# Performance work log

Measured on AMD Instinct MI355X. Metric: run time of the kernel, lower is better.

Reference implementation:

```python
import jax, jax.numpy as jnp
import numpy as np

C2D, C3D = 256, 128
IA, IB = C2D // 2, C3D // 2  # inter channels: 128, 64
B, H, W = 4, 64, 64


def _conv1x1(x, w, b):
    # x: [B,Cin,H,W], w: [Cout,Cin], b: [Cout]
    return jnp.einsum('oc,bchw->bohw', w, x) + b[None, :, None, None]


def _cross_attn(Q, K, V):
    # Q,K,V: [B,C,H,W] (same C); full HWxHW attention as in the torch code
    Bs, C, h, w = Q.shape
    q = Q.reshape(Bs, C, h * w)
    k = K.reshape(Bs, C, K.shape[2] * K.shape[3])
    v = V.reshape(Bs, C, V.shape[2] * V.shape[3])
    attn = jnp.einsum('bcn,bcm->bnm', q, k) * (C ** -0.5)  # [B,N,M]
    attn = jax.nn.softmax(attn, axis=-1)
    out = jnp.einsum('bnm,bcm->bcn', attn, v)
    return out.reshape(Bs, C, h, w)


def setup_inputs() -> dict:
    key = jax.random.key(0)
    ks = jax.random.split(key, 20)
    def n(k, shape, scale=0.02):
        return jax.random.normal(k, shape, dtype=jnp.float32) * scale
    inp = {
        'features_2d': jax.random.normal(ks[0], (B, C2D, H, W), dtype=jnp.float32),
        'features_3d': jax.random.normal(ks[1], (B, C3D, H, W), dtype=jnp.float32),
        # stream A: Q from 2d, K/V from 3d, all mapped to IA channels
        'wqA': n(ks[2], (IA, C2D)), 'bqA': jnp.zeros((IA,), jnp.float32),
        'wkA': n(ks[3], (IA, C3D)), 'bkA': jnp.zeros((IA,), jnp.float32),
        'wvA': n(ks[4], (IA, C3D)), 'bvA': jnp.zeros((IA,), jnp.float32),
        'wpA': n(ks[5], (C2D, IA)), 'bpA': jnp.zeros((C2D,), jnp.float32),
        # stream B: Q from 3d, K/V from 2d, all mapped to IB channels
        'wqB': n(ks[6], (IB, C3D)), 'bqB': jnp.zeros((IB,), jnp.float32),
        'wkB': n(ks[7], (IB, C2D)), 'bkB': jnp.zeros((IB,), jnp.float32),
        'wvB': n(ks[8], (IB, C2D)), 'bvB': jnp.zeros((IB,), jnp.float32),
        'wpB': n(ks[9], (C3D, IB)), 'bpB': jnp.zeros((C3D,), jnp.float32),
    }
    return inp


def reference(features_2d, features_3d,
              wqA, bqA, wkA, bkA, wvA, bvA, wpA, bpA,
              wqB, bqB, wkB, bkB, wvB, bvB, wpB, bpB):
    Q_A = _conv1x1(features_2d, wqA, bqA)
    K_A = _conv1x1(features_3d, wkA, bkA)
    V_A = _conv1x1(features_3d, wvA, bvA)
    x_2D = features_2d + _conv1x1(_cross_attn(Q_A, K_A, V_A), wpA, bpA)

    Q_B = _conv1x1(features_3d, wqB, bqB)
    K_B = _conv1x1(features_2d, wkB, bkB)
    V_B = _conv1x1(features_2d, wvB, bvB)
    x_3D = features_3d + _conv1x1(_cross_attn(Q_B, K_B, V_B), wpB, bpB)
    return (x_2D, x_3D)
```

## Files before the change

### kernel.cpp

```cpp
#include <hip/hip_runtime.h>
#include <hip/hip_bf16.h>
#include <math.h>

typedef __bf16 bf16_t;
typedef __bf16 bf16x8 __attribute__((ext_vector_type(8)));
typedef float f32x4 __attribute__((ext_vector_type(4)));
typedef float f32x16 __attribute__((ext_vector_type(16)));
typedef unsigned u32x2 __attribute__((ext_vector_type(2)));

#define NPOS 4096
#define LOG2E 1.4426950408889634f

__device__ __forceinline__ f32x4 mfma16(bf16x8 a, bf16x8 b, f32x4 c) {
    return __builtin_amdgcn_mfma_f32_16x16x32_bf16(a, b, c, 0, 0, 0);
}
__device__ __forceinline__ f32x16 mfma32(bf16x8 a, bf16x8 b, f32x16 c) {
    return __builtin_amdgcn_mfma_f32_32x32x16_bf16(a, b, c, 0, 0, 0);
}

typedef __attribute__((address_space(1))) const unsigned gas_u32;
typedef __attribute__((address_space(3))) unsigned las_u32;
__device__ __forceinline__ void gl_lds16(const char* g, char* l) {
    __builtin_amdgcn_global_load_lds((gas_u32*)g, (las_u32*)l, 16, 0, 0);
}

__device__ __forceinline__ float fexp2(float x) {
    float r; asm("v_exp_f32 %0, %1" : "=v"(r) : "v"(x)); return r;
}

#define BARC(N) do {                                                          \
    asm volatile("s_waitcnt vmcnt(" #N ") lgkmcnt(0)" ::: "memory");          \
    __builtin_amdgcn_sched_barrier(0);                                        \
    __builtin_amdgcn_s_barrier();                                             \
    __builtin_amdgcn_sched_barrier(0);                                        \
} while (0)

template<int BYTES>
__device__ __forceinline__ void stG(char* lds, const char* g, int w, int lane) {
    constexpr int NC = BYTES / 4096;
#pragma unroll
    for (int c = 0; c < NC; ++c) {
        int j = (w * NC + c) * 1024 + lane * 16;
        gl_lds16(g + (j ^ (((j >> 8) & 15) << 4)), lds + j);
    }
}
template<int BYTES>
__device__ __forceinline__ void stV(char* lds, const char* g, int w, int lane) {
    constexpr int NC = BYTES / 4096;
#pragma unroll
    for (int c = 0; c < NC; ++c) {
        int j = (w * NC + c) * 1024 + lane * 16;
        int row = j >> 8;
        int col = (j & 255) ^ ((row & 15) << 4);
        int d = (row << 1) | (col >> 7);
        gl_lds16(g + (size_t)d * (NPOS * 2) + (col & 127), lds + j);
    }
}

template<int D>
__device__ __forceinline__ bf16x8 ldK(const char* lds, int key, int dbyte) {
    if constexpr (D == 128) {
        return *(const bf16x8*)(lds + key * 256 + (dbyte ^ ((key & 15) << 4)));
    } else {
        int row = key >> 1;
        int col = ((key & 1) << 7) | dbyte;
        return *(const bf16x8*)(lds + row * 256 + (col ^ ((row & 15) << 4)));
    }
}
__device__ __forceinline__ bf16x8 ldV(const char* lds, int d, int kbyte) {
    int row = d >> 1;
    int col = ((d & 1) << 7) | kbyte;
    return *(const bf16x8*)(lds + row * 256 + (col ^ ((row & 15) << 4)));
}

__device__ __forceinline__ unsigned pkbf(float a, float b) {
    union { bf16_t h[2]; unsigned u; } t;
    t.h[0] = (bf16_t)a; t.h[1] = (bf16_t)b;
    return t.u;
}
#define MKPA(sb, base) ({                                                   \
    unsigned a0_ = pkbf((sb)[(base)+0], (sb)[(base)+1]);                    \
    unsigned a1_ = pkbf((sb)[(base)+2], (sb)[(base)+3]);                    \
    unsigned a2_ = pkbf((sb)[(base)+4], (sb)[(base)+5]);                    \
    unsigned a3_ = pkbf((sb)[(base)+6], (sb)[(base)+7]);                    \
    u32x2 r0_ = __builtin_amdgcn_permlane32_swap(a2_, a0_, false, false);   \
    u32x2 r1_ = __builtin_amdgcn_permlane32_swap(a3_, a1_, false, false);   \
    union { unsigned u[4]; bf16x8 v; } pu_;                                 \
    pu_.u[0] = r0_.y; pu_.u[1] = r1_.y; pu_.u[2] = r0_.x; pu_.u[3] = r1_.x; \
    pu_.v; })

__global__ __launch_bounds__(256) void k_trw(const float* __restrict__ s2d,
                                             const float* __restrict__ s3d,
                                             bf16_t* __restrict__ d2d,
                                             bf16_t* __restrict__ d3d,
                                             const float* w0, const float* w1, const float* w2, const float* w3,
                                             const float* w4, const float* w5, const float* w6, const float* w7,
                                             bf16_t* wdst)
{
    __shared__ float tile[64][65];
    int bid = blockIdx.x, tid = threadIdx.x;
    if (bid >= 1536) {
        int i = (bid - 1536) * 256 + tid;
        if      (i <  32768) wdst[i] = (bf16_t)w0[i];
        else if (i <  49152) wdst[i] = (bf16_t)w1[i - 32768];
        else if (i <  65536) wdst[i] = (bf16_t)w2[i - 49152];
        else if (i <  98304) wdst[i] = (bf16_t)w3[i - 65536];
        else if (i < 106496) wdst[i] = (bf16_t)w4[i - 98304];
        else if (i < 122880) wdst[i] = (bf16_t)w5[i - 106496];
        else if (i < 139264) wdst[i] = (bf16_t)w6[i - 122880];
        else if (i < 147456) wdst[i] = (bf16_t)w7[i - 139264];
        return;
    }
    const float* src; bf16_t* dst; int C, b, c0, n0;
    if (bid < 1024) { src = s2d; dst = d2d; C = 256; b = bid >> 8; c0 = ((bid >> 6) & 3) << 6; n0 = (bid & 63) << 6; }
    else { int r = bid - 1024; src = s3d; dst = d3d; C = 128; b = r >> 7; c0 = ((r >> 6) & 1) << 6; n0 = (r & 63) << 6; }
    const float* sp = src + ((size_t)b * C + c0) * NPOS + n0;
#pragma unroll
    for (int i = 0; i < 16; i++) {
        int idx = tid + i * 256; int c = idx >> 6, n = idx & 63;
        tile[c][n] = sp[(size_t)c * NPOS + n];
    }
    __syncthreads();
    bf16_t* dp = dst + ((size_t)b * NPOS + n0) * C + c0;
#pragma unroll
    for (int i = 0; i < 16; i++) {
        int idx = tid + i * 256; int n = idx >> 6, c = idx & 63;
        dp[(size_t)n * C + c] = (bf16_t)tile[c][n];
    }
}

template<int K, int MQ, int MK, int MV>
__global__ __launch_bounds__(256, 2) void k_prod(const bf16_t* __restrict__ Xt,
                                                 const bf16_t* __restrict__ wq, const float* __restrict__ bq, float sq,
                                                 const bf16_t* __restrict__ wk, const float* __restrict__ bk,
                                                 const bf16_t* __restrict__ wv, const float* __restrict__ bv,
                                                 bf16_t* __restrict__ Qo, bf16_t* __restrict__ Ko, bf16_t* __restrict__ Vo)
{
    extern __shared__ char smem[];
    constexpr int RB = K * 2;
    int bid = blockIdx.x, tid = threadIdx.x;
    int b = bid >> 6, n0 = (bid & 63) << 6;
    int wave = tid >> 6, lane = tid & 63, g = lane >> 4, lr = lane & 15;

    const char* src = (const char*)(Xt + ((size_t)b * NPOS + n0) * K);
#pragma unroll
    for (int j0 = 0; j0 < 64 * RB; j0 += 4096) {
        int j = j0 + tid * 16;
        int row = j / RB;
        int col = j & (RB - 1);
        float4 v = *(const float4*)(src + (size_t)row * RB + col);
        *(float4*)(smem + row * RB + (col ^ ((row & 7) << 4))) = v;
    }
    __syncthreads();

    f32x4 aq[MQ / 16], ak[MK / 16], av[MV / 16];
#pragma unroll
    for (int ob = 0; ob < MQ / 16; ++ob) aq[ob] = f32x4{0.f,0.f,0.f,0.f};
#pragma unroll
    for (int ob = 0; ob < MK / 16; ++ob) ak[ob] = f32x4{0.f,0.f,0.f,0.f};
#pragma unroll
    for (int ob = 0; ob < MV / 16; ++ob) av[ob] = f32x4{0.f,0.f,0.f,0.f};
    int xrow = wave * 16 + lr;
#pragma unroll
    for (int ks = 0; ks < K / 32; ++ks) {
        bf16x8 xf = *(const bf16x8*)(smem + xrow * RB + ((((ks * 32 + g * 8) * 2)) ^ ((xrow & 7) << 4)));
#pragma unroll
        for (int ob = 0; ob < MQ / 16; ++ob) {
            bf16x8 wf = *(const bf16x8*)(wq + (size_t)(ob * 16 + lr) * K + ks * 32 + g * 8);
            aq[ob] = mfma16(xf, wf, aq[ob]);
        }
#pragma unroll
        for (int ob = 0; ob < MK / 16; ++ob) {
            bf16x8 wf = *(const bf16x8*)(wk + (size_t)(ob * 16 + lr) * K + ks * 32 + g * 8);
            ak[ob] = mfma16(xf, wf, ak[ob]);
        }
#pragma unroll
        for (int ob = 0; ob < MV / 16; ++ob) {
            bf16x8 wf = *(const bf16x8*)(wv + (size_t)(ob * 16 + lr) * K + ks * 32 + g * 8);
            av[ob] = mfma16(wf, xf, av[ob]);
        }
    }
#pragma unroll
    for (int ob = 0; ob < MQ / 16; ++ob) {
        int o = ob * 16 + lr;
        float bs = bq[o];
#pragma unroll
        for (int r = 0; r < 4; r++) {
            size_t n = (size_t)b * NPOS + n0 + wave * 16 + g * 4 + r;
            Qo[n * MQ + o] = (bf16_t)((aq[ob][r] + bs) * sq);
        }
    }
#pragma unroll
    for (int ob = 0; ob < MK / 16; ++ob) {
        int o = ob * 16 + lr;
        float bs = bk[o];
#pragma unroll
        for (int r = 0; r < 4; r++) {
            size_t n = (size_t)b * NPOS + n0 + wave * 16 + g * 4 + r;
            Ko[n * MK + o] = (bf16_t)(ak[ob][r] + bs);
        }
    }
#pragma unroll
    for (int ob = 0; ob < MV / 16; ++ob) {
#pragma unroll
        for (int r = 0; r < 4; r++) {
            int o = ob * 16 + g * 4 + r;
            size_t idx = ((size_t)b * MV + o) * NPOS + n0 + wave * 16 + lr;
            Vo[idx] = (bf16_t)(av[ob][r] + bv[o]);
        }
    }
}

template<int K, int M>
__global__ __launch_bounds__(256, 2) void k_out(const bf16_t* __restrict__ Xt,
                                                const bf16_t* __restrict__ W,
                                                const float* __restrict__ bias,
                                                const float* __restrict__ resid,
                                                float* __restrict__ outp,
                                                const float* __restrict__ lp)
{
    extern __shared__ char smem[];
    constexpr int RB = K * 2;
    int bid = blockIdx.x, tid = threadIdx.x;
    int b = bid >> 6, n0 = (bid & 63) << 6;
    int wave = tid >> 6, lane = tid & 63, g = lane >> 4, lr = lane & 15;

#pragma unroll
    for (int j0 = 0; j0 < 64 * RB; j0 += 4096) {
        int j = j0 + tid * 16;
        int row = j / RB;
        int colb = j & (RB - 1);
        size_t n = (size_t)b * NPOS + n0 + row;
        float l1 = lp[n], l2 = lp[16384 + n];
        float inv = 1.f / (l1 + l2);
        float w1 = l1 * inv, w2 = l2 * inv;
        bf16x8 o1 = *(const bf16x8*)(Xt + n * K + (colb >> 1));
        bf16x8 o2 = *(const bf16x8*)(Xt + (size_t)16384 * K + n * K + (colb >> 1));
        bf16x8 xv;
#pragma unroll
        for (int e = 0; e < 8; ++e) xv[e] = (bf16_t)(w1 * (float)o1[e] + w2 * (float)o2[e]);
        *(bf16x8*)(smem + row * RB + (colb ^ ((row & 7) << 4))) = xv;
    }
    __syncthreads();

    f32x4 acc[M / 16];
#pragma unroll
    for (int ob = 0; ob < M / 16; ++ob) acc[ob] = f32x4{0.f,0.f,0.f,0.f};
    int xrow = wave * 16 + lr;
#pragma unroll
    for (int ks = 0; ks < K / 32; ++ks) {
        bf16x8 xf = *(const bf16x8*)(smem + xrow * RB + ((((ks * 32 + g * 8) * 2)) ^ ((xrow & 7) << 4)));
#pragma unroll
        for (int ob = 0; ob < M / 16; ++ob) {
            bf16x8 wf = *(const bf16x8*)(W + (size_t)(ob * 16 + lr) * K + ks * 32 + g * 8);
            acc[ob] = mfma16(wf, xf, acc[ob]);
        }
    }
#pragma unroll
    for (int ob = 0; ob < M / 16; ++ob) {
#pragma unroll
        for (int r = 0; r < 4; r++) {
            int o = ob * 16 + g * 4 + r;
            size_t idx = ((size_t)b * M + o) * NPOS + n0 + wave * 16 + lr;
            outp[idx] = acc[ob][r] + bias[o] + resid[idx];
        }
    }
}

__device__ void attnA9(const bf16_t* __restrict__ Qt, const bf16_t* __restrict__ Kt,
                       const bf16_t* __restrict__ V, bf16_t* __restrict__ OtH,
                       float* __restrict__ lH, int b, int qblk, int half,
                       char* smem, int tid)
{
    char* Kb[3] = { smem, smem + 8192, smem + 16384 };
    char* Vb[2] = { smem + 24576, smem + 40960 };
    int w = tid >> 6, lane = tid & 63;
    int qcol = lane & 31, hi = lane >> 5;
    int q0 = qblk * 128 + w * 32;

    bf16x8 qf[8];
    const bf16_t* qp = Qt + ((size_t)b * NPOS + q0 + qcol) * 128 + hi * 8;
#pragma unroll
    for (int ks = 0; ks < 8; ++ks) qf[ks] = *(const bf16x8*)(qp + ks * 16);

    f32x16 acc[4];
#pragma unroll
    for (int cb = 0; cb < 4; ++cb)
#pragma unroll
        for (int i = 0; i < 16; ++i) acc[cb][i] = 0.f;
    float l_c = 0.f;

    const char* kg = (const char*)(Kt + (size_t)b * NPOS * 128) + (size_t)half * 64 * 8192;
    const char* vg = (const char*)(V + (size_t)b * 128 * NPOS) + (size_t)half * 32 * 128;

    stG<8192>(Kb[0], kg, w, lane);
    stV<16384>(Vb[0], vg, w, lane);
    stG<8192>(Kb[1], kg + 8192, w, lane);
    BARC(2);

    int rc = 0;
#pragma unroll 1
    for (int t2 = 0; t2 < 32; ++t2) {
        {
            int tK = 2 * t2 + 2; if (tK > 63) tK = 63;
            int st1 = t2 + 1;    if (st1 > 31) st1 = 31;
            int wn = rc ? rc - 1 : 2;
            stG<8192>(Kb[wn], kg + (size_t)tK * 8192, w, lane);
            stV<16384>(Vb[(t2 + 1) & 1], vg + (size_t)st1 * 128, w, lane);
            const char* Kc = Kb[rc];
            const char* Vc = Vb[t2 & 1];

            f32x16 s;
#pragma unroll
            for (int i = 0; i < 16; ++i) s[i] = 0.f;
            __builtin_amdgcn_s_setprio(1);
#pragma unroll
            for (int ks = 0; ks < 8; ++ks)
                s = mfma32(ldK<128>(Kc, qcol, ks * 32 + hi * 16), qf[ks], s);
            __builtin_amdgcn_s_setprio(0);
            float psum = 0.f;
#pragma unroll
            for (int i = 0; i < 16; ++i) { float e = fexp2(s[i]); s[i] = e; psum += e; }
            psum += __shfl_xor(psum, 32);
            l_c += psum;
            bf16x8 pa0 = MKPA(s, 0);
            bf16x8 pa1 = MKPA(s, 8);
            __builtin_amdgcn_s_setprio(1);
#pragma unroll
            for (int cb = 0; cb < 4; ++cb) {
                int d = cb * 32 + qcol;
                acc[cb] = mfma32(pa0, ldV(Vc, d, 0 + hi * 16), acc[cb]);
                acc[cb] = mfma32(pa1, ldV(Vc, d, 32 + hi * 16), acc[cb]);
            }
            __builtin_amdgcn_s_setprio(0);
            rc = (rc == 2) ? 0 : rc + 1;
            BARC(6);
        }
        {
            int tK = 2 * t2 + 3; if (tK > 63) tK = 63;
            int wn = rc ? rc - 1 : 2;
            stG<8192>(Kb[wn], kg + (size_t)tK * 8192, w, lane);
            const char* Kc = Kb[rc];
            const char* Vc = Vb[t2 & 1];

            f32x16 s;
#pragma unroll
            for (int i = 0; i < 16; ++i) s[i] = 0.f;
            __builtin_amdgcn_s_setprio(1);
#pragma unroll
            for (int ks = 0; ks < 8; ++ks)
                s = mfma32(ldK<128>(Kc, qcol, ks * 32 + hi * 16), qf[ks], s);
            __builtin_amdgcn_s_setprio(0);
            float psum = 0.f;
#pragma unroll
            for (int i = 0; i < 16; ++i) { float e = fexp2(s[i]); s[i] = e; psum += e; }
            psum += __shfl_xor(psum, 32);
            l_c += psum;
            bf16x8 pa0 = MKPA(s, 0);
            bf16x8 pa1 = MKPA(s, 8);
            __builtin_amdgcn_s_setprio(1);
#pragma unroll
            for (int cb = 0; cb < 4; ++cb) {
                int d = cb * 32 + qcol;
                acc[cb] = mfma32(pa0, ldV(Vc, d, 64 + hi * 16), acc[cb]);
                acc[cb] = mfma32(pa1, ldV(Vc, d, 96 + hi * 16), acc[cb]);
            }
            __builtin_amdgcn_s_setprio(0);
            rc = (rc == 2) ? 0 : rc + 1;
            BARC(2);
        }
    }

    float linv = 1.f / l_c;
    size_t obase = (size_t)(half * 4 + b) * NPOS;
#pragma unroll
    for (int r = 0; r < 16; ++r) {
        int crow = (r & 3) + 8 * (r >> 2) + 4 * hi;
        float lr = __shfl(linv, crow);
        size_t nrow = obase + q0 + crow;
#pragma unroll
        for (int cb = 0; cb < 4; ++cb)
            OtH[nrow * 128 + cb * 32 + qcol] = (bf16_t)(acc[cb][r] * lr);
    }
    if (lane < 32) lH[obase + q0 + lane] = l_c;
}

__device__ void attnB9(const bf16_t* __restrict__ Qt, const bf16_t* __restrict__ Kt,
                       const bf16_t* __restrict__ V, bf16_t* __restrict__ OtH,
                       float* __restrict__ lH, int b, int qblk, int half,
                       char* smem, int tid)
{
    char* Kb[3] = { smem, smem + 8192, smem + 16384 };
    char* Vb[3] = { smem + 24576, smem + 32768, smem + 40960 };
    int w = tid >> 6, lane = tid & 63;
    int qcol = lane & 31, hi = lane >> 5;
    int q0 = qblk * 128 + w * 32;

    bf16x8 qf[4];
    const bf16_t* qp = Qt + ((size_t)b * NPOS + q0 + qcol) * 64 + hi * 8;
#pragma unroll
    for (int ks = 0; ks < 4; ++ks) qf[ks] = *(const bf16x8*)(qp + ks * 16);

    f32x16 acc[2];
#pragma unroll
    for (int cb = 0; cb < 2; ++cb)
#pragma unroll
        for (int i = 0; i < 16; ++i) acc[cb][i] = 0.f;
    float l_c = 0.f;

    const char* kg = (const char*)(Kt + (size_t)b * NPOS * 64) + (size_t)half * 32 * 8192;
    const char* vg = (const char*)(V + (size_t)b * 64 * NPOS) + (size_t)half * 4096;

    stG<8192>(Kb[0], kg, w, lane);
    stV<8192>(Vb[0], vg, w, lane);
    stG<8192>(Kb[1], kg + 8192, w, lane);
    stV<8192>(Vb[1], vg + 128, w, lane);
    BARC(4);

    int rc = 0;
#pragma unroll 1
    for (int t = 0; t < 32; ++t) {
        int tn = t + 2; if (tn > 31) tn = 31;
        int wn = rc ? rc - 1 : 2;
        stG<8192>(Kb[wn], kg + (size_t)tn * 8192, w, lane);
        stV<8192>(Vb[wn], vg + (size_t)tn * 128, w, lane);
        const char* Kc = Kb[rc];
        const char* Vc = Vb[rc];

        f32x16 s0, s1;
#pragma unroll
        for (int i = 0; i < 16; ++i) { s0[i] = 0.f; s1[i] = 0.f; }
        __builtin_amdgcn_s_setprio(1);
#pragma unroll
        for (int ks = 0; ks < 4; ++ks) {
            int dbyte = ks * 32 + hi * 16;
            s0 = mfma32(ldK<64>(Kc, qcol, dbyte), qf[ks], s0);
            s1 = mfma32(ldK<64>(Kc, 32 + qcol, dbyte), qf[ks], s1);
        }
        __builtin_amdgcn_s_setprio(0);

        float psum = 0.f;
#pragma unroll
        for (int i = 0; i < 16; ++i) { float e = fexp2(s0[i]); s0[i] = e; psum += e; }
#pragma unroll
        for (int i = 0; i < 16; ++i) { float e = fexp2(s1[i]); s1[i] = e; psum += e; }
        psum += __shfl_xor(psum, 32);
        l_c += psum;

        bf16x8 pa0 = MKPA(s0, 0);
        bf16x8 pa1 = MKPA(s0, 8);
        bf16x8 pa2 = MKPA(s1, 0);
        bf16x8 pa3 = MKPA(s1, 8);

        __builtin_amdgcn_s_setprio(1);
#pragma unroll
        for (int cb = 0; cb < 2; ++cb) {
            int d = cb * 32 + qcol;
            acc[cb] = mfma32(pa0, ldV(Vc, d, 0  + hi * 16), acc[cb]);
            acc[cb] = mfma32(pa1, ldV(Vc, d, 32 + hi * 16), acc[cb]);
            acc[cb] = mfma32(pa2, ldV(Vc, d, 64 + hi * 16), acc[cb]);
            acc[cb] = mfma32(pa3, ldV(Vc, d, 96 + hi * 16), acc[cb]);
        }
        __builtin_amdgcn_s_setprio(0);
        rc = (rc == 2) ? 0 : rc + 1;
        BARC(4);
    }

    float linv = 1.f / l_c;
    size_t obase = (size_t)(half * 4 + b) * NPOS;
#pragma unroll
    for (int r = 0; r < 16; ++r) {
        int crow = (r & 3) + 8 * (r >> 2) + 4 * hi;
        float lr = __shfl(linv, crow);
        size_t nrow = obase + q0 + crow;
#pragma unroll
        for (int cb = 0; cb < 2; ++cb)
            OtH[nrow * 64 + cb * 32 + qcol] = (bf16_t)(acc[cb][r] * lr);
    }
    if (lane < 32) lH[obase + q0 + lane] = l_c;
}

__global__ __launch_bounds__(256, 2) void k_attn9(const bf16_t* QtA, const bf16_t* KtA, const bf16_t* VA,
                                                  bf16_t* OtHA, float* lHA,
                                                  const bf16_t* QtB, const bf16_t* KtB, const bf16_t* VB,
                                                  bf16_t* OtHB, float* lHB)
{
    extern __shared__ char smem[];
    int bid = blockIdx.x, tid = threadIdx.x;
    if (bid < 256) {
        int x = bid & 7;
        attnA9(QtA, KtA, VA, OtHA, lHA, x >> 1, bid >> 3, x & 1, smem, tid);
    } else {
        int u = bid - 256;
        int x = u & 7;
        attnB9(QtB, KtB, VB, OtHB, lHB, x >> 1, u >> 3, x & 1, smem, tid);
    }
}

extern "C" void kernel_launch(void* const* d_in, const int* in_sizes, int n_in,
                              void* d_out, int out_size, void* d_ws, size_t ws_size,
                              hipStream_t stream)
{
    (void)in_sizes; (void)n_in; (void)out_size; (void)ws_size;
    const float* f2d = (const float*)d_in[0];
    const float* f3d = (const float*)d_in[1];
    const float* wqA = (const float*)d_in[2];  const float* bqA = (const float*)d_in[3];
    const float* wkA = (const float*)d_in[4];  const float* bkA = (const float*)d_in[5];
    const float* wvA = (const float*)d_in[6];  const float* bvA = (const float*)d_in[7];
    const float* wpA = (const float*)d_in[8];  const float* bpA = (const float*)d_in[9];
    const float* wqB = (const float*)d_in[10]; const float* bqB = (const float*)d_in[11];
    const float* wkB = (const float*)d_in[12]; const float* bkB = (const float*)d_in[13];
    const float* wvB = (const float*)d_in[14]; const float* bvB = (const float*)d_in[15];
    const float* wpB = (const float*)d_in[16]; const float* bpB = (const float*)d_in[17];

    char* ws = (char*)d_ws;
    bf16_t* ft2d = (bf16_t*)(ws);
    bf16_t* ft3d = (bf16_t*)(ws + 8388608);
    bf16_t* wbf  = (bf16_t*)(ws + 12582912);
    bf16_t* QtA  = (bf16_t*)(ws + 12877824);
    bf16_t* KtA_ = (bf16_t*)(ws + 17072128);
    bf16_t* VA_  = (bf16_t*)(ws + 21266432);
    bf16_t* QtB  = (bf16_t*)(ws + 25460736);
    bf16_t* KtB_ = (bf16_t*)(ws + 27557888);
    bf16_t* VB_  = (bf16_t*)(ws + 29655040);
    bf16_t* OtHA = (bf16_t*)(ws);
    float*  lHA  = (float*)(ws + 8388608);
    bf16_t* OtHB = (bf16_t*)(ws + 31752192);
    float*  lHB  = (float*)(ws + 35946496);

    k_trw<<<2112, 256, 0, stream>>>(f2d, f3d, ft2d, ft3d,
                                    wqA, wkA, wvA, wpA, wqB, wkB, wvB, wpB, wbf);

    const float sA = 0.08838834764831845f * LOG2E;
    const float sB = 0.125f * LOG2E;

    k_prod<256, 128, 64, 64><<<256, 256, 32768, stream>>>(ft2d,
        wbf + 0, bqA, sA, wbf + 106496, bkB, wbf + 122880, bvB, QtA, KtB_, VB_);
    k_prod<128, 64, 128, 128><<<256, 256, 16384, stream>>>(ft3d,
        wbf + 98304, bqB, sB, wbf + 32768, bkA, wbf + 49152, bvA, QtB, KtA_, VA_);

    k_attn9<<<512, 256, 57344, stream>>>(QtA, KtA_, VA_, OtHA, lHA, QtB, KtB_, VB_, OtHB, lHB);

    k_out<128, 256><<<256, 256, 16384, stream>>>(OtHA, wbf + 65536, bpA, f2d, (float*)d_out, lHA);
    k_out<64, 128><<<256, 256, 8192, stream>>>(OtHB, wbf + 139264, bpB, f3d, (float*)d_out + 4194304, lHB);
}
```

Before: 146.8 us.

## Process two query tiles per wave in stream-A attention with 4-way key split

Each wave in stream-A attention now handles 64 queries as two 32-row tiles. Every K and V fragment loaded from LDS feeds two MFMAs, which halves LDS traffic per unit of work. To keep the block count the same, the keys are split four ways instead of two. The four partial outputs and row sums are merged in a new output-projection kernel that weights each partial by its row sum. This raises register pressure (doubled accumulators and Q fragments) and adds workspace traffic for the extra partials.

```diff
diff --git a/kernel.cpp b/kernel.cpp
--- a/kernel.cpp
+++ b/kernel.cpp
@@ -267,31 +267,129 @@
     }
 }
 
-__device__ void attnA9(const bf16_t* __restrict__ Qt, const bf16_t* __restrict__ Kt,
-                       const bf16_t* __restrict__ V, bf16_t* __restrict__ OtH,
-                       float* __restrict__ lH, int b, int qblk, int half,
-                       char* smem, int tid)
+__global__ __launch_bounds__(256, 2) void k_outA(const bf16_t* __restrict__ Xt,
+                                                 const bf16_t* __restrict__ Xt3,
+                                                 const bf16_t* __restrict__ W,
+                                                 const float* __restrict__ bias,
+                                                 const float* __restrict__ resid,
+                                                 float* __restrict__ outp,
+                                                 const float* __restrict__ lp)
+{
+    extern __shared__ char smem[];
+    constexpr int K = 128, M = 256, RB = 256;
+    int bid = blockIdx.x, tid = threadIdx.x;
+    int b = bid >> 6, n0 = (bid & 63) << 6;
+    int wave = tid >> 6, lane = tid & 63, g = lane >> 4, lr = lane & 15;
+
+#pragma unroll
+    for (int j0 = 0; j0 < 64 * RB; j0 += 4096) {
+        int j = j0 + tid * 16;
+        int row = j >> 8;
+        int colb = j & 255;
+        size_t n = (size_t)b * NPOS + n0 + row;
+        float l0 = lp[n], l1 = lp[16384 + n], l2 = lp[32768 + n], l3 = lp[49152 + n];
+        float inv = 1.f / (l0 + l1 + l2 + l3);
+        bf16x8 o0 = *(const bf16x8*)(Xt  + (size_t)0 * 2097152 + n * K + (colb >> 1));
+        bf16x8 o1 = *(const bf16x8*)(Xt  + (size_t)1 * 2097152 + n * K + (colb >> 1));
+        bf16x8 o2 = *(const bf16x8*)(Xt  + (size_t)2 * 2097152 + n * K + (colb >> 1));
+        bf16x8 o3 = *(const bf16x8*)(Xt3 + n * K + (colb >> 1));
+        float w0 = l0 * inv, w1 = l1 * inv, w2 = l2 * inv, w3 = l3 * inv;
+        bf16x8 xv;
+#pragma unroll
+        for (int e = 0; e < 8; ++e)
+            xv[e] = (bf16_t)(w0 * (float)o0[e] + w1 * (float)o1[e] + w2 * (float)o2[e] + w3 * (float)o3[e]);
+        *(bf16x8*)(smem + row * RB + (colb ^ ((row & 7) << 4))) = xv;
+    }
+    __syncthreads();
+
+    f32x4 acc[M / 16];
+#pragma unroll
+    for (int ob = 0; ob < M / 16; ++ob) acc[ob] = f32x4{0.f,0.f,0.f,0.f};
+    int xrow = wave * 16 + lr;
+#pragma unroll
+    for (int ks = 0; ks < K / 32; ++ks) {
+        bf16x8 xf = *(const bf16x8*)(smem + xrow * RB + ((((ks * 32 + g * 8) * 2)) ^ ((xrow & 7) << 4)));
+#pragma unroll
+        for (int ob = 0; ob < M / 16; ++ob) {
+            bf16x8 wf = *(const bf16x8*)(W + (size_t)(ob * 16 + lr) * K + ks * 32 + g * 8);
+            acc[ob] = mfma16(wf, xf, acc[ob]);
+        }
+    }
+#pragma unroll
+    for (int ob = 0; ob < M / 16; ++ob) {
+#pragma unroll
+        for (int r = 0; r < 4; r++) {
+            int o = ob * 16 + g * 4 + r;
+            size_t idx = ((size_t)b * M + o) * NPOS + n0 + wave * 16 + lr;
+            outp[idx] = acc[ob][r] + bias[o] + resid[idx];
+        }
+    }
+}
+
+__device__ void attnA10(const bf16_t* __restrict__ Qt, const bf16_t* __restrict__ Kt,
+                        const bf16_t* __restrict__ V, bf16_t* __restrict__ Op,
+                        float* __restrict__ lH, int b, int qblk, int split,
+                        char* smem, int tid)
 {
     char* Kb[3] = { smem, smem + 8192, smem + 16384 };
     char* Vb[2] = { smem + 24576, smem + 40960 };
     int w = tid >> 6, lane = tid & 63;
     int qcol = lane & 31, hi = lane >> 5;
-    int q0 = qblk * 128 + w * 32;
-
-    bf16x8 qf[8];
-    const bf16_t* qp = Qt + ((size_t)b * NPOS + q0 + qcol) * 128 + hi * 8;
-#pragma unroll
-    for (int ks = 0; ks < 8; ++ks) qf[ks] = *(const bf16x8*)(qp + ks * 16);
-
-    f32x16 acc[4];
+    int q0 = qblk * 256 + w * 64;
+
+    bf16x8 qfa[8], qfb[8];
+    const bf16_t* qpa = Qt + ((size_t)b * NPOS + q0 + qcol) * 128 + hi * 8;
+#pragma unroll
+    for (int ks = 0; ks < 8; ++ks) {
+        qfa[ks] = *(const bf16x8*)(qpa + ks * 16);
+        qfb[ks] = *(const bf16x8*)(qpa + 32 * 128 + ks * 16);
+    }
+
+    f32x16 aa[4], ab[4];
 #pragma unroll
     for (int cb = 0; cb < 4; ++cb)
 #pragma unroll
-        for (int i = 0; i < 16; ++i) acc[cb][i] = 0.f;
-    float l_c = 0.f;
-
-    const char* kg = (const char*)(Kt + (size_t)b * NPOS * 128) + (size_t)half * 64 * 8192;
-    const char* vg = (const char*)(V + (size_t)b * 128 * NPOS) + (size_t)half * 32 * 128;
+        for (int i = 0; i < 16; ++i) { aa[cb][i] = 0.f; ab[cb][i] = 0.f; }
+    float la = 0.f, lb = 0.f;
+
+    const char* kg = (const char*)(Kt + (size_t)b * NPOS * 128) + (size_t)split * 262144;
+    const char* vg = (const char*)(V + (size_t)b * 128 * NPOS) + (size_t)split * 2048;
+
+    auto body = [&](const char* Kc, const char* Vc, int kb) {
+        f32x16 sa, sb;
+#pragma unroll
+        for (int i = 0; i < 16; ++i) { sa[i] = 0.f; sb[i] = 0.f; }
+        __builtin_amdgcn_s_setprio(1);
+#pragma unroll
+        for (int ks = 0; ks < 8; ++ks) {
+            bf16x8 kf = ldK<128>(Kc, qcol, ks * 32 + hi * 16);
+            sa = mfma32(kf, qfa[ks], sa);
+            sb = mfma32(kf, qfb[ks], sb);
+        }
+        __builtin_amdgcn_s_setprio(0);
+        float pa_ = 0.f, pb_ = 0.f;
+#pragma unroll
+        for (int i = 0; i < 16; ++i) { float e = fexp2(sa[i]); sa[i] = e; pa_ += e; }
+#pragma unroll
+        for (int i = 0; i < 16; ++i) { float e = fexp2(sb[i]); sb[i] = e; pb_ += e; }
+        pa_ += __shfl_xor(pa_, 32);
+        pb_ += __shfl_xor(pb_, 32);
+        la += pa_; lb += pb_;
+        bf16x8 Aa0 = MKPA(sa, 0), Aa1 = MKPA(sa, 8);
+        bf16x8 Ab0 = MKPA(sb, 0), Ab1 = MKPA(sb, 8);
+        __builtin_amdgcn_s_setprio(1);
+#pragma unroll
+        for (int cb = 0; cb < 4; ++cb) {
+            int d = cb * 32 + qcol;
+            bf16x8 v0 = ldV(Vc, d, kb + hi * 16);
+            bf16x8 v1 = ldV(Vc, d, kb + 32 + hi * 16);
+            aa[cb] = mfma32(Aa0, v0, aa[cb]);
+            ab[cb] = mfma32(Ab0, v0, ab[cb]);
+            aa[cb] = mfma32(Aa1, v1, aa[cb]);
+            ab[cb] = mfma32(Ab1, v1, ab[cb]);
+        }
+        __builtin_amdgcn_s_setprio(0);
+    };
 
     stG<8192>(Kb[0], kg, w, lane);
     stV<16384>(Vb[0], vg, w, lane);
@@ -300,89 +398,46 @@
 
     int rc = 0;
 #pragma unroll 1
-    for (int t2 = 0; t2 < 32; ++t2) {
+    for (int t2 = 0; t2 < 16; ++t2) {
         {
-            int tK = 2 * t2 + 2; if (tK > 63) tK = 63;
-            int st1 = t2 + 1;    if (st1 > 31) st1 = 31;
+            int tK = 2 * t2 + 2; if (tK > 31) tK = 31;
+            int st1 = t2 + 1;    if (st1 > 15) st1 = 15;
             int wn = rc ? rc - 1 : 2;
             stG<8192>(Kb[wn], kg + (size_t)tK * 8192, w, lane);
             stV<16384>(Vb[(t2 + 1) & 1], vg + (size_t)st1 * 128, w, lane);
-            const char* Kc = Kb[rc];
-            const char* Vc = Vb[t2 & 1];
-
-            f32x16 s;
-#pragma unroll
-            for (int i = 0; i < 16; ++i) s[i] = 0.f;
-            __builtin_amdgcn_s_setprio(1);
-#pragma unroll
-            for (int ks = 0; ks < 8; ++ks)
-                s = mfma32(ldK<128>(Kc, qcol, ks * 32 + hi * 16), qf[ks], s);
-            __builtin_amdgcn_s_setprio(0);
-            float psum = 0.f;
-#pragma unroll
-            for (int i = 0; i < 16; ++i) { float e = fexp2(s[i]); s[i] = e; psum += e; }
-            psum += __shfl_xor(psum, 32);
-            l_c += psum;
-            bf16x8 pa0 = MKPA(s, 0);
-            bf16x8 pa1 = MKPA(s, 8);
-            __builtin_amdgcn_s_setprio(1);
-#pragma unroll
-            for (int cb = 0; cb < 4; ++cb) {
-                int d = cb * 32 + qcol;
-                acc[cb] = mfma32(pa0, ldV(Vc, d, 0 + hi * 16), acc[cb]);
-                acc[cb] = mfma32(pa1, ldV(Vc, d, 32 + hi * 16), acc[cb]);
-            }
-            __builtin_amdgcn_s_setprio(0);
+            body(Kb[rc], Vb[t2 & 1], 0);
             rc = (rc == 2) ? 0 : rc + 1;
             BARC(6);
         }
         {
-            int tK = 2 * t2 + 3; if (tK > 63) tK = 63;
+            int tK = 2 * t2 + 3; if (tK > 31) tK = 31;
             int wn = rc ? rc - 1 : 2;
             stG<8192>(Kb[wn], kg + (size_t)tK * 8192, w, lane);
-            const char* Kc = Kb[rc];
-            const char* Vc = Vb[t2 & 1];
-
-            f32x16 s;
-#pragma unroll
-            for (int i = 0; i < 16; ++i) s[i] = 0.f;
-            __builtin_amdgcn_s_setprio(1);
-#pragma unroll
-            for (int ks = 0; ks < 8; ++ks)
-                s = mfma32(ldK<128>(Kc, qcol, ks * 32 + hi * 16), qf[ks], s);
-            __builtin_amdgcn_s_setprio(0);
-            float psum = 0.f;
-#pragma unroll
-            for (int i = 0; i < 16; ++i) { float e = fexp2(s[i]); s[i] = e; psum += e; }
-            psum += __shfl_xor(psum, 32);
-            l_c += psum;
-            bf16x8 pa0 = MKPA(s, 0);
-            bf16x8 pa1 = MKPA(s, 8);
-            __builtin_amdgcn_s_setprio(1);
-#pragma unroll
-            for (int cb = 0; cb < 4; ++cb) {
-                int d = cb * 32 + qcol;
-                acc[cb] = mfma32(pa0, ldV(Vc, d, 64 + hi * 16), acc[cb]);
-                acc[cb] = mfma32(pa1, ldV(Vc, d, 96 + hi * 16), acc[cb]);
-            }
-            __builtin_amdgcn_s_setprio(0);
+            body(Kb[rc], Vb[t2 & 1], 64);
             rc = (rc == 2) ? 0 : rc + 1;
             BARC(2);
         }
     }
 
-    float linv = 1.f / l_c;
-    size_t obase = (size_t)(half * 4 + b) * NPOS;
+    float ia = 1.f / la, ib = 1.f / lb;
+    size_t obase = (size_t)b * NPOS + q0;
 #pragma unroll
     for (int r = 0; r < 16; ++r) {
         int crow = (r & 3) + 8 * (r >> 2) + 4 * hi;
-        float lr = __shfl(linv, crow);
-        size_t nrow = obase + q0 + crow;
-#pragma unroll
-        for (int cb = 0; cb < 4; ++cb)
-            OtH[nrow * 128 + cb * 32 + qcol] = (bf16_t)(acc[cb][r] * lr);
-    }
-    if (lane < 32) lH[obase + q0 + lane] = l_c;
+        float ga = __shfl(ia, crow);
+        float gb = __shfl(ib, crow);
+        size_t na = obase + crow, nb = obase + 32 + crow;
+#pragma unroll
+        for (int cb = 0; cb < 4; ++cb) {
+            Op[na * 128 + cb * 32 + qcol] = (bf16_t)(aa[cb][r] * ga);
+            Op[nb * 128 + cb * 32 + qcol] = (bf16_t)(ab[cb][r] * gb);
+        }
+    }
+    int loff = split * 16384 + b * NPOS + q0;
+    if (lane < 32) {
+        lH[loff + lane] = la;
+        lH[loff + 32 + lane] = lb;
+    }
 }
 
 __device__ void attnB9(const bf16_t* __restrict__ Qt, const bf16_t* __restrict__ Kt,
@@ -480,16 +535,18 @@
     if (lane < 32) lH[obase + q0 + lane] = l_c;
 }
 
-__global__ __launch_bounds__(256, 2) void k_attn9(const bf16_t* QtA, const bf16_t* KtA, const bf16_t* VA,
-                                                  bf16_t* OtHA, float* lHA,
-                                                  const bf16_t* QtB, const bf16_t* KtB, const bf16_t* VB,
-                                                  bf16_t* OtHB, float* lHB)
+__global__ __launch_bounds__(256, 2) void k_attn10(const bf16_t* QtA, const bf16_t* KtA, const bf16_t* VA,
+                                                   bf16_t* OtHA, bf16_t* OtHA3, float* lHA,
+                                                   const bf16_t* QtB, const bf16_t* KtB, const bf16_t* VB,
+                                                   bf16_t* OtHB, float* lHB)
 {
     extern __shared__ char smem[];
     int bid = blockIdx.x, tid = threadIdx.x;
     if (bid < 256) {
-        int x = bid & 7;
-        attnA9(QtA, KtA, VA, OtHA, lHA, x >> 1, bid >> 3, x & 1, smem, tid);
+        int x = bid & 7, u = bid >> 3;
+        int b = x >> 1, split = (x & 1) * 2 + (u & 1), qblk = u >> 1;
+        bf16_t* op = (split < 3) ? OtHA + (size_t)split * 2097152 : OtHA3;
+        attnA10(QtA, KtA, VA, op, lHA, b, qblk, split, smem, tid);
     } else {
         int u = bid - 256;
         int x = u & 7;
@@ -523,10 +580,11 @@
     bf16_t* QtB  = (bf16_t*)(ws + 25460736);
     bf16_t* KtB_ = (bf16_t*)(ws + 27557888);
     bf16_t* VB_  = (bf16_t*)(ws + 29655040);
-    bf16_t* OtHA = (bf16_t*)(ws);
-    float*  lHA  = (float*)(ws + 8388608);
     bf16_t* OtHB = (bf16_t*)(ws + 31752192);
     float*  lHB  = (float*)(ws + 35946496);
+    bf16_t* OtHA  = (bf16_t*)(ws);
+    bf16_t* OtHA3 = (bf16_t*)(ws + 36077568);
+    float*  lHA   = (float*)(ws + 40271872);
 
     k_trw<<<2112, 256, 0, stream>>>(f2d, f3d, ft2d, ft3d,
                                     wqA, wkA, wvA, wpA, wqB, wkB, wvB, wpB, wbf);
@@ -539,8 +597,9 @@
     k_prod<128, 64, 128, 128><<<256, 256, 16384, stream>>>(ft3d,
         wbf + 98304, bqB, sB, wbf + 32768, bkA, wbf + 49152, bvA, QtB, KtA_, VA_);
 
-    k_attn9<<<512, 256, 57344, stream>>>(QtA, KtA_, VA_, OtHA, lHA, QtB, KtB_, VB_, OtHB, lHB);
-
-    k_out<128, 256><<<256, 256, 16384, stream>>>(OtHA, wbf + 65536, bpA, f2d, (float*)d_out, lHA);
+    k_attn10<<<512, 256, 57344, stream>>>(QtA, KtA_, VA_, OtHA, OtHA3, lHA,
+                                          QtB, KtB_, VB_, OtHB, lHB);
+
+    k_outA<<<256, 256, 16384, stream>>>(OtHA, OtHA3, wbf + 65536, bpA, f2d, (float*)d_out, lHA);
     k_out<64, 128><<<256, 256, 8192, stream>>>(OtHB, wbf + 139264, bpB, f3d, (float*)d_out + 4194304, lHB);
 }
```

Measured after the change: 217.6 us. 48.2% more time.

## Software-pipeline QK^T of next tile with softmax/PV of current tile

Applied to the files above, without the earlier changes.

Both attention streams now compute the QK^T scores for the next key tile before doing the exp/sum and PV MFMAs for the current tile, so the exp work can overlap with tensor-core work. Stream A's V staging moves from 16KB double buffers to 8KB triple buffers per 64-key tile (new stV32/ldV32 layout), which cuts dynamic LDS from 57344 to 49152 bytes. The change adds register pressure from keeping two score tiles live and adds runtime buffer selection through sel3.

```diff
diff --git a/kernel.cpp b/kernel.cpp
--- a/kernel.cpp
+++ b/kernel.cpp
@@ -35,6 +35,10 @@
     __builtin_amdgcn_sched_barrier(0);                                        \
 } while (0)
 
+__device__ __forceinline__ char* sel3(char* a, char* b, char* c, int i) {
+    return i == 0 ? a : (i == 1 ? b : c);
+}
+
 template<int BYTES>
 __device__ __forceinline__ void stG(char* lds, const char* g, int w, int lane) {
     constexpr int NC = BYTES / 4096;
@@ -54,6 +58,18 @@
         int col = (j & 255) ^ ((row & 15) << 4);
         int d = (row << 1) | (col >> 7);
         gl_lds16(g + (size_t)d * (NPOS * 2) + (col & 127), lds + j);
+    }
+}
+template<int BYTES>
+__device__ __forceinline__ void stV32(char* lds, const char* g, int w, int lane) {
+    constexpr int NC = BYTES / 4096;
+#pragma unroll
+    for (int c = 0; c < NC; ++c) {
+        int j = (w * NC + c) * 1024 + lane * 16;
+        int row = j >> 8;
+        int col = (j & 255) ^ ((row & 15) << 4);
+        int d = (row << 2) | (col >> 6);
+        gl_lds16(g + (size_t)d * (NPOS * 2) + (col & 63), lds + j);
     }
 }
 
@@ -70,6 +86,11 @@
 __device__ __forceinline__ bf16x8 ldV(const char* lds, int d, int kbyte) {
     int row = d >> 1;
     int col = ((d & 1) << 7) | kbyte;
+    return *(const bf16x8*)(lds + row * 256 + (col ^ ((row & 15) << 4)));
+}
+__device__ __forceinline__ bf16x8 ldV32(const char* lds, int d, int kbyte) {
+    int row = d >> 2;
+    int col = ((d & 3) << 6) | kbyte;
     return *(const bf16x8*)(lds + row * 256 + (col ^ ((row & 15) << 4)));
 }
 
@@ -267,13 +288,13 @@
     }
 }
 
-__device__ void attnA9(const bf16_t* __restrict__ Qt, const bf16_t* __restrict__ Kt,
-                       const bf16_t* __restrict__ V, bf16_t* __restrict__ OtH,
-                       float* __restrict__ lH, int b, int qblk, int half,
-                       char* smem, int tid)
+__device__ void attnA11(const bf16_t* __restrict__ Qt, const bf16_t* __restrict__ Kt,
+                        const bf16_t* __restrict__ V, bf16_t* __restrict__ OtH,
+                        float* __restrict__ lH, int b, int qblk, int half,
+                        char* smem, int tid)
 {
-    char* Kb[3] = { smem, smem + 8192, smem + 16384 };
-    char* Vb[2] = { smem + 24576, smem + 40960 };
+    char* Kb0 = smem;          char* Kb1 = smem + 8192;  char* Kb2 = smem + 16384;
+    char* Vb0 = smem + 24576;  char* Vb1 = smem + 32768; char* Vb2 = smem + 40960;
     int w = tid >> 6, lane = tid & 63;
     int qcol = lane & 31, hi = lane >> 5;
     int q0 = qblk * 128 + w * 32;
@@ -291,84 +312,90 @@
     float l_c = 0.f;
 
     const char* kg = (const char*)(Kt + (size_t)b * NPOS * 128) + (size_t)half * 64 * 8192;
-    const char* vg = (const char*)(V + (size_t)b * 128 * NPOS) + (size_t)half * 32 * 128;
-
-    stG<8192>(Kb[0], kg, w, lane);
-    stV<16384>(Vb[0], vg, w, lane);
-    stG<8192>(Kb[1], kg + 8192, w, lane);
+    const char* vg = (const char*)(V + (size_t)b * 128 * NPOS) + (size_t)half * 4096;
+
+    stG<8192>(Kb0, kg, w, lane);
+    stV32<8192>(Vb0, vg, w, lane);
+    stG<8192>(Kb1, kg + 8192, w, lane);
+    stV32<8192>(Vb1, vg + 64, w, lane);
+    BARC(4);
+
+    f32x16 sE, sO;
+#pragma unroll
+    for (int i = 0; i < 16; ++i) sE[i] = 0.f;
+#pragma unroll
+    for (int ks = 0; ks < 8; ++ks)
+        sE = mfma32(ldK<128>(Kb0, qcol, ks * 32 + hi * 16), qf[ks], sE);
+    stG<8192>(Kb2, kg + 16384, w, lane);
     BARC(2);
 
-    int rc = 0;
+    int ce = 0;
 #pragma unroll 1
     for (int t2 = 0; t2 < 32; ++t2) {
+        int t = 2 * t2;
+        int c1 = ce + 1; if (c1 > 2) c1 -= 3;
+        int c2 = ce + 2; if (c2 > 2) c2 -= 3;
         {
-            int tK = 2 * t2 + 2; if (tK > 63) tK = 63;
-            int st1 = t2 + 1;    if (st1 > 31) st1 = 31;
-            int wn = rc ? rc - 1 : 2;
-            stG<8192>(Kb[wn], kg + (size_t)tK * 8192, w, lane);
-            stV<16384>(Vb[(t2 + 1) & 1], vg + (size_t)st1 * 128, w, lane);
-            const char* Kc = Kb[rc];
-            const char* Vc = Vb[t2 & 1];
-
-            f32x16 s;
-#pragma unroll
-            for (int i = 0; i < 16; ++i) s[i] = 0.f;
+            int tK = t + 3; if (tK > 63) tK = 63;
+            int tV = t + 2; if (tV > 63) tV = 63;
+            stG<8192>(sel3(Kb0, Kb1, Kb2, ce), kg + (size_t)tK * 8192, w, lane);
+            stV32<8192>(sel3(Vb0, Vb1, Vb2, c2), vg + (size_t)tV * 64, w, lane);
+            const char* Kn = sel3(Kb0, Kb1, Kb2, c1);
+#pragma unroll
+            for (int i = 0; i < 16; ++i) sO[i] = 0.f;
             __builtin_amdgcn_s_setprio(1);
 #pragma unroll
             for (int ks = 0; ks < 8; ++ks)
-                s = mfma32(ldK<128>(Kc, qcol, ks * 32 + hi * 16), qf[ks], s);
-            __builtin_amdgcn_s_setprio(0);
-            float psum = 0.f;
-#pragma unroll
-            for (int i = 0; i < 16; ++i) { float e = fexp2(s[i]); s[i] = e; psum += e; }
-            psum += __shfl_xor(psum, 32);
-            l_c += psum;
-            bf16x8 pa0 = MKPA(s, 0);
-            bf16x8 pa1 = MKPA(s, 8);
+                sO = mfma32(ldK<128>(Kn, qcol, ks * 32 + hi * 16), qf[ks], sO);
+            __builtin_amdgcn_s_setprio(0);
+            float ps = 0.f;
+#pragma unroll
+            for (int i = 0; i < 16; ++i) { float e = fexp2(sE[i]); sE[i] = e; ps += e; }
+            ps += __shfl_xor(ps, 32);
+            l_c += ps;
+            bf16x8 pa0 = MKPA(sE, 0), pa1 = MKPA(sE, 8);
+            const char* Vc = sel3(Vb0, Vb1, Vb2, ce);
             __builtin_amdgcn_s_setprio(1);
 #pragma unroll
             for (int cb = 0; cb < 4; ++cb) {
                 int d = cb * 32 + qcol;
-                acc[cb] = mfma32(pa0, ldV(Vc, d, 0 + hi * 16), acc[cb]);
-                acc[cb] = mfma32(pa1, ldV(Vc, d, 32 + hi * 16), acc[cb]);
+                acc[cb] = mfma32(pa0, ldV32(Vc, d, hi * 16), acc[cb]);
+                acc[cb] = mfma32(pa1, ldV32(Vc, d, 32 + hi * 16), acc[cb]);
             }
             __builtin_amdgcn_s_setprio(0);
-            rc = (rc == 2) ? 0 : rc + 1;
-            BARC(6);
+            BARC(4);
         }
         {
-            int tK = 2 * t2 + 3; if (tK > 63) tK = 63;
-            int wn = rc ? rc - 1 : 2;
-            stG<8192>(Kb[wn], kg + (size_t)tK * 8192, w, lane);
-            const char* Kc = Kb[rc];
-            const char* Vc = Vb[t2 & 1];
-
-            f32x16 s;
-#pragma unroll
-            for (int i = 0; i < 16; ++i) s[i] = 0.f;
+            int tK = t + 4; if (tK > 63) tK = 63;
+            int tV = t + 3; if (tV > 63) tV = 63;
+            stG<8192>(sel3(Kb0, Kb1, Kb2, c1), kg + (size_t)tK * 8192, w, lane);
+            stV32<8192>(sel3(Vb0, Vb1, Vb2, ce), vg + (size_t)tV * 64, w, lane);
+            const char* Kn = sel3(Kb0, Kb1, Kb2, c2);
+#pragma unroll
+            for (int i = 0; i < 16; ++i) sE[i] = 0.f;
             __builtin_amdgcn_s_setprio(1);
 #pragma unroll
             for (int ks = 0; ks < 8; ++ks)
-                s = mfma32(ldK<128>(Kc, qcol, ks * 32 + hi * 16), qf[ks], s);
-            __builtin_amdgcn_s_setprio(0);
-            float psum = 0.f;
-#pragma unroll
-            for (int i = 0; i < 16; ++i) { float e = fexp2(s[i]); s[i] = e; psum += e; }
-            psum += __shfl_xor(psum, 32);
-            l_c += psum;
-            bf16x8 pa0 = MKPA(s, 0);
-            bf16x8 pa1 = MKPA(s, 8);
+                sE = mfma32(ldK<128>(Kn, qcol, ks * 32 + hi * 16), qf[ks], sE);
+            __builtin_amdgcn_s_setprio(0);
+            float ps = 0.f;
+#pragma unroll
+            for (int i = 0; i < 16; ++i) { float e = fexp2(sO[i]); sO[i] = e; ps += e; }
+            ps += __shfl_xor(ps, 32);
+            l_c += ps;
+            bf16x8 pa0 = MKPA(sO, 0), pa1 = MKPA(sO, 8);
+            const char* Vc = sel3(Vb0, Vb1, Vb2, c1);
             __builtin_amdgcn_s_setprio(1);
 #pragma unroll
             for (int cb = 0; cb < 4; ++cb) {
                 int d = cb * 32 + qcol;
-                acc[cb] = mfma32(pa0, ldV(Vc, d, 64 + hi * 16), acc[cb]);
-                acc[cb] = mfma32(pa1, ldV(Vc, d, 96 + hi * 16), acc[cb]);
+                acc[cb] = mfma32(pa0, ldV32(Vc, d, hi * 16), acc[cb]);
+                acc[cb] = mfma32(pa1, ldV32(Vc, d, 32 + hi * 16), acc[cb]);
             }
             __builtin_amdgcn_s_setprio(0);
-            rc = (rc == 2) ? 0 : rc + 1;
-            BARC(2);
-        }
+            BARC(4);
+        }
+        ce = c2;
     }
 
     float linv = 1.f / l_c;
@@ -385,13 +412,13 @@
     if (lane < 32) lH[obase + q0 + lane] = l_c;
 }
 
-__device__ void attnB9(const bf16_t* __restrict__ Qt, const bf16_t* __restrict__ Kt,
-                       const bf16_t* __restrict__ V, bf16_t* __restrict__ OtH,
-                       float* __restrict__ lH, int b, int qblk, int half,
-                       char* smem, int tid)
+__device__ void attnB11(const bf16_t* __restrict__ Qt, const bf16_t* __restrict__ Kt,
+                        const bf16_t* __restrict__ V, bf16_t* __restrict__ OtH,
+                        float* __restrict__ lH, int b, int qblk, int half,
+                        char* smem, int tid)
 {
-    char* Kb[3] = { smem, smem + 8192, smem + 16384 };
-    char* Vb[3] = { smem + 24576, smem + 32768, smem + 40960 };
+    char* Kb0 = smem;          char* Kb1 = smem + 8192;  char* Kb2 = smem + 16384;
+    char* Vb0 = smem + 24576;  char* Vb1 = smem + 32768; char* Vb2 = smem + 40960;
     int w = tid >> 6, lane = tid & 63;
     int qcol = lane & 31, hi = lane >> 5;
     int q0 = qblk * 128 + w * 32;
@@ -411,59 +438,107 @@
     const char* kg = (const char*)(Kt + (size_t)b * NPOS * 64) + (size_t)half * 32 * 8192;
     const char* vg = (const char*)(V + (size_t)b * 64 * NPOS) + (size_t)half * 4096;
 
-    stG<8192>(Kb[0], kg, w, lane);
-    stV<8192>(Vb[0], vg, w, lane);
-    stG<8192>(Kb[1], kg + 8192, w, lane);
-    stV<8192>(Vb[1], vg + 128, w, lane);
+    stG<8192>(Kb0, kg, w, lane);
+    stV<8192>(Vb0, vg, w, lane);
+    stG<8192>(Kb1, kg + 8192, w, lane);
+    stV<8192>(Vb1, vg + 128, w, lane);
     BARC(4);
 
-    int rc = 0;
+    f32x16 sE0, sE1, sO0, sO1;
+#pragma unroll
+    for (int i = 0; i < 16; ++i) { sE0[i] = 0.f; sE1[i] = 0.f; }
+#pragma unroll
+    for (int ks = 0; ks < 4; ++ks) {
+        int dbyte = ks * 32 + hi * 16;
+        sE0 = mfma32(ldK<64>(Kb0, qcol, dbyte), qf[ks], sE0);
+        sE1 = mfma32(ldK<64>(Kb0, 32 + qcol, dbyte), qf[ks], sE1);
+    }
+    stG<8192>(Kb2, kg + 16384, w, lane);
+    BARC(2);
+
+    int ce = 0;
 #pragma unroll 1
-    for (int t = 0; t < 32; ++t) {
-        int tn = t + 2; if (tn > 31) tn = 31;
-        int wn = rc ? rc - 1 : 2;
-        stG<8192>(Kb[wn], kg + (size_t)tn * 8192, w, lane);
-        stV<8192>(Vb[wn], vg + (size_t)tn * 128, w, lane);
-        const char* Kc = Kb[rc];
-        const char* Vc = Vb[rc];
-
-        f32x16 s0, s1;
-#pragma unroll
-        for (int i = 0; i < 16; ++i) { s0[i] = 0.f; s1[i] = 0.f; }
-        __builtin_amdgcn_s_setprio(1);
-#pragma unroll
-        for (int ks = 0; ks < 4; ++ks) {
-            int dbyte = ks * 32 + hi * 16;
-            s0 = mfma32(ldK<64>(Kc, qcol, dbyte), qf[ks], s0);
-            s1 = mfma32(ldK<64>(Kc, 32 + qcol, dbyte), qf[ks], s1);
-        }
-        __builtin_amdgcn_s_setprio(0);
-
-        float psum = 0.f;
-#pragma unroll
-        for (int i = 0; i < 16; ++i) { float e = fexp2(s0[i]); s0[i] = e; psum += e; }
-#pragma unroll
-        for (int i = 0; i < 16; ++i) { float e = fexp2(s1[i]); s1[i] = e; psum += e; }
-        psum += __shfl_xor(psum, 32);
-        l_c += psum;
-
-        bf16x8 pa0 = MKPA(s0, 0);
-        bf16x8 pa1 = MKPA(s0, 8);
-        bf16x8 pa2 = MKPA(s1, 0);
-        bf16x8 pa3 = MKPA(s1, 8);
-
-        __builtin_amdgcn_s_setprio(1);
-#pragma unroll
-        for (int cb = 0; cb < 2; ++cb) {
-            int d = cb * 32 + qcol;
-            acc[cb] = mfma32(pa0, ldV(Vc, d, 0  + hi * 16), acc[cb]);
-            acc[cb] = mfma32(pa1, ldV(Vc, d, 32 + hi * 16), acc[cb]);
-            acc[cb] = mfma32(pa2, ldV(Vc, d, 64 + hi * 16), acc[cb]);
-            acc[cb] = mfma32(pa3, ldV(Vc, d, 96 + hi * 16), acc[cb]);
-        }
-        __builtin_amdgcn_s_setprio(0);
-        rc = (rc == 2) ? 0 : rc + 1;
-        BARC(4);
+    for (int t2 = 0; t2 < 16; ++t2) {
+        int t = 2 * t2;
+        int c1 = ce + 1; if (c1 > 2) c1 -= 3;
+        int c2 = ce + 2; if (c2 > 2) c2 -= 3;
+        {
+            int tK = t + 3; if (tK > 31) tK = 31;
+            int tV = t + 2; if (tV > 31) tV = 31;
+            stG<8192>(sel3(Kb0, Kb1, Kb2, ce), kg + (size_t)tK * 8192, w, lane);
+            stV<8192>(sel3(Vb0, Vb1, Vb2, c2), vg + (size_t)tV * 128, w, lane);
+            const char* Kn = sel3(Kb0, Kb1, Kb2, c1);
+#pragma unroll
+            for (int i = 0; i < 16; ++i) { sO0[i] = 0.f; sO1[i] = 0.f; }
+            __builtin_amdgcn_s_setprio(1);
+#pragma unroll
+            for (int ks = 0; ks < 4; ++ks) {
+                int dbyte = ks * 32 + hi * 16;
+                sO0 = mfma32(ldK<64>(Kn, qcol, dbyte), qf[ks], sO0);
+                sO1 = mfma32(ldK<64>(Kn, 32 + qcol, dbyte), qf[ks], sO1);
+            }
+            __builtin_amdgcn_s_setprio(0);
+            float ps = 0.f;
+#pragma unroll
+            for (int i = 0; i < 16; ++i) { float e = fexp2(sE0[i]); sE0[i] = e; ps += e; }
+#pragma unroll
+            for (int i = 0; i < 16; ++i) { float e = fexp2(sE1[i]); sE1[i] = e; ps += e; }
+            ps += __shfl_xor(ps, 32);
+            l_c += ps;
+            bf16x8 pa0 = MKPA(sE0, 0), pa1 = MKPA(sE0, 8);
+            bf16x8 pa2 = MKPA(sE1, 0), pa3 = MKPA(sE1, 8);
+            const char* Vc = sel3(Vb0, Vb1, Vb2, ce);
+            __builtin_amdgcn_s_setprio(1);
+#pragma unroll
+            for (int cb = 0; cb < 2; ++cb) {
+                int d = cb * 32 + qcol;
+                acc[cb] = mfma32(pa0, ldV(Vc, d, 0  + hi * 16), acc[cb]);
+                acc[cb] = mfma32(pa1, ldV(Vc, d, 32 + hi * 16), acc[cb]);
+                acc[cb] = mfma32(pa2, ldV(Vc, d, 64 + hi * 16), acc[cb]);
+                acc[cb] = mfma32(pa3, ldV(Vc, d, 96 + hi * 16), acc[cb]);
+            }
+            __builtin_amdgcn_s_setprio(0);
+            BARC(4);
+        }
+        {
+            int tK = t + 4; if (tK > 31) tK = 31;
+            int tV = t + 3; if (tV > 31) tV = 31;
+            stG<8192>(sel3(Kb0, Kb1, Kb2, c1), kg + (size_t)tK * 8192, w, lane);
+            stV<8192>(sel3(Vb0, Vb1, Vb2, ce), vg + (size_t)tV * 128, w, lane);
+            const char* Kn = sel3(Kb0, Kb1, Kb2, c2);
+#pragma unroll
+            for (int i = 0; i < 16; ++i) { sE0[i] = 0.f; sE1[i] = 0.f; }
+            __builtin_amdgcn_s_setprio(1);
+#pragma unroll
+            for (int ks = 0; ks < 4; ++ks) {
+                int dbyte = ks * 32 + hi * 16;
+                sE0 = mfma32(ldK<64>(Kn, qcol, dbyte), qf[ks], sE0);
+                sE1 = mfma32(ldK<64>(Kn, 32 + qcol, dbyte), qf[ks], sE1);
+            }
+            __builtin_amdgcn_s_setprio(0);
+            float ps = 0.f;
+#pragma unroll
+            for (int i = 0; i < 16; ++i) { float e = fexp2(sO0[i]); sO0[i] = e; ps += e; }
+#pragma unroll
+            for (int i = 0; i < 16; ++i) { float e = fexp2(sO1[i]); sO1[i] = e; ps += e; }
+            ps += __shfl_xor(ps, 32);
+            l_c += ps;
+            bf16x8 pa0 = MKPA(sO0, 0), pa1 = MKPA(sO0, 8);
+            bf16x8 pa2 = MKPA(sO1, 0), pa3 = MKPA(sO1, 8);
+            const char* Vc = sel3(Vb0, Vb1, Vb2, c1);
+            __builtin_amdgcn_s_setprio(1);
+#pragma unroll
+            for (int cb = 0; cb < 2; ++cb) {
+                int d = cb * 32 + qcol;
+                acc[cb] = mfma32(pa0, ldV(Vc, d, 0  + hi * 16), acc[cb]);
+                acc[cb] = mfma32(pa1, ldV(Vc, d, 32 + hi * 16), acc[cb]);
+                acc[cb] = mfma32(pa2, ldV(Vc, d, 64 + hi * 16), acc[cb]);
+                acc[cb] = mfma32(pa3, ldV(Vc, d, 96 + hi * 16), acc[cb]);
+            }
+            __builtin_amdgcn_s_setprio(0);
+            BARC(4);
+        }
+        ce = c2;
     }
 
     float linv = 1.f / l_c;
@@ -480,20 +555,20 @@
     if (lane < 32) lH[obase + q0 + lane] = l_c;
 }
 
-__global__ __launch_bounds__(256, 2) void k_attn9(const bf16_t* QtA, const bf16_t* KtA, const bf16_t* VA,
-                                                  bf16_t* OtHA, float* lHA,
-                                                  const bf16_t* QtB, const bf16_t* KtB, const bf16_t* VB,
-                                                  bf16_t* OtHB, float* lHB)
+__global__ __launch_bounds__(256, 2) void k_attn11(const bf16_t* QtA, const bf16_t* KtA, const bf16_t* VA,
+                                                   bf16_t* OtHA, float* lHA,
+                                                   const bf16_t* QtB, const bf16_t* KtB, const bf16_t* VB,
+                                                   bf16_t* OtHB, float* lHB)
 {
     extern __shared__ char smem[];
     int bid = blockIdx.x, tid = threadIdx.x;
     if (bid < 256) {
         int x = bid & 7;
-        attnA9(QtA, KtA, VA, OtHA, lHA, x >> 1, bid >> 3, x & 1, smem, tid);
+        attnA11(QtA, KtA, VA, OtHA, lHA, x >> 1, bid >> 3, x & 1, smem, tid);
     } else {
         int u = bid - 256;
         int x = u & 7;
-        attnB9(QtB, KtB, VB, OtHB, lHB, x >> 1, u >> 3, x & 1, smem, tid);
+        attnB11(QtB, KtB, VB, OtHB, lHB, x >> 1, u >> 3, x & 1, smem, tid);
     }
 }
 
@@ -539,7 +614,7 @@
     k_prod<128, 64, 128, 128><<<256, 256, 16384, stream>>>(ft3d,
         wbf + 98304, bqB, sB, wbf + 32768, bkA, wbf + 49152, bvA, QtB, KtA_, VA_);
 
-    k_attn9<<<512, 256, 57344, stream>>>(QtA, KtA_, VA_, OtHA, lHA, QtB, KtB_, VB_, OtHB, lHB);
+    k_attn11<<<512, 256, 49152, stream>>>(QtA, KtA_, VA_, OtHA, lHA, QtB, KtB_, VB_, OtHB, lHB);
 
     k_out<128, 256><<<256, 256, 16384, stream>>>(OtHA, wbf + 65536, bpA, f2d, (float*)d_out, lHA);
     k_out<64, 128><<<256, 256, 8192, stream>>>(OtHB, wbf + 139264, bpB, f3d, (float*)d_out + 4194304, lHB);
```

Result: faster. 129.3 us (-11.9%).
